# Performance work log

Hardware: AMD Instinct MI355X
Metric: run time of the kernel (lower is better)

## Reference

```python
import jax, jax.numpy as jnp
import numpy as np


def setup_inputs() -> dict:
    key = jax.random.key(0)
    ks = jax.random.split(key, 6)
    B, H, W, C = 4, 64, 64, 256
    D = 256 // 4  # inter_channel // 4
    return {
        "g": jax.random.normal(ks[0], (B, H, W, C), dtype=jnp.float32),
        "x": jax.random.normal(ks[1], (B, H, W, C), dtype=jnp.float32),
        "x_query": jax.random.normal(ks[2], (B, H, W, D), dtype=jnp.float32),
        "phi_g": jax.random.normal(ks[3], (B, H, W, D), dtype=jnp.float32),
        "x_value": jax.random.normal(ks[4], (B, H, W, C), dtype=jnp.float32),
        "k": jax.random.normal(ks[5], (1,), dtype=jnp.float32),
    }


def reference(g, x, x_query, phi_g, x_value, k):
    B, H, W, C = x.shape
    D = x_query.shape[-1]
    HW = H * W
    q = x_query.reshape(B, HW, D)
    pg = phi_g.reshape(B, HW, D)
    v = x_value.reshape(B, HW, C)
    # scale[b,i,j] = sum_d phi_g[b,i,d] * x_query[b,j,d]  -> (B, HW, HW)
    scale = jnp.einsum("bid,bjd->bij", pg, q)
    soft = jax.nn.softmax(scale, axis=-1)
    # scaled_value[b,i,c] = sum_j soft[b,i,j] * v[b,j,c]
    sv = jnp.einsum("bij,bjc->bic", soft, v).reshape(B, H, W, C)
    layero = k * sv + x
    return jnp.concatenate([layero, g], axis=3)
```

## Files before the change

kernel.cpp:

```cpp
#include <hip/hip_runtime.h>

#define N_  4096
#define D_  64
#define C_  256

typedef short bf16x8 __attribute__((ext_vector_type(8)));
typedef float f32x4  __attribute__((ext_vector_type(4)));

__device__ __forceinline__ unsigned short f2bf(float f) {
    union { float f; unsigned int i; } v; v.f = f;
    unsigned int r = v.i + 0x7fffu + ((v.i >> 16) & 1u);
    return (unsigned short)(r >> 16);
}

__global__ void prepass_kernel(const float* __restrict__ xq,
                               const float* __restrict__ pg,
                               const float* __restrict__ xv,
                               unsigned short* __restrict__ qbf,
                               unsigned short* __restrict__ pgbf,
                               unsigned short* __restrict__ vt2) {
    const int bid = blockIdx.x;
    const int t   = threadIdx.x;
    if (bid < 512) {
        const float* src = (bid < 256) ? xq : pg;
        unsigned short* dst = (bid < 256) ? qbf : pgbf;
        const int base = (bid & 255) * 1024 + t;
#pragma unroll
        for (int it = 0; it < 4; ++it) {
            const int i = base + it * 256;
            float4 v = ((const float4*)src)[i];
            ushort4 o;
            o.x = f2bf(v.x); o.y = f2bf(v.y); o.z = f2bf(v.z); o.w = f2bf(v.w);
            ((ushort4*)dst)[i] = o;
        }
        return;
    }
    const int lane = t & 63;
    const int w    = t >> 6;
    const int l15  = lane & 15;
    const int quad = lane >> 4;
    const int f    = (bid - 512) * 4 + w;
    const int b    = f >> 11;
    const int jt   = (f >> 6) & 31;
    const int cb   = (f >> 2) & 15;
    const int ks   = f & 3;
    const int c    = cb * 16 + l15;
    const int jb   = jt * 128 + ks * 32 + quad * 8;
    const float* src = xv + ((size_t)b * N_ + jb) * C_ + c;
    float v0 = src[0 * C_], v1 = src[1 * C_], v2 = src[2 * C_], v3 = src[3 * C_];
    float v4 = src[4 * C_], v5 = src[5 * C_], v6 = src[6 * C_], v7 = src[7 * C_];
    uint4 o;
    o.x = (unsigned)f2bf(v0) | ((unsigned)f2bf(v1) << 16);
    o.y = (unsigned)f2bf(v2) | ((unsigned)f2bf(v3) << 16);
    o.z = (unsigned)f2bf(v4) | ((unsigned)f2bf(v5) << 16);
    o.w = (unsigned)f2bf(v6) | ((unsigned)f2bf(v7) << 16);
    *(uint4*)(vt2 + (size_t)f * 512 + lane * 8) = o;
}

__global__ __launch_bounds__(512, 2) void attn_main(
    const float* __restrict__ g,  const float* __restrict__ x,
    const float* __restrict__ kk, float* __restrict__ out,
    const unsigned short* __restrict__ qbf,
    const unsigned short* __restrict__ pgbf,
    const unsigned short* __restrict__ vt2)
{
    __shared__ unsigned short p_lds[2][64 * 128];
    __shared__ float s_l[64];

    const int t    = threadIdx.x;
    const int lane = t & 63;
    const int w    = t >> 6;
    const int l15  = lane & 15;
    const int quad = lane >> 4;
    const int swz  = (l15 & 7) << 4;

    const int bid = blockIdx.x;
    const int b   = bid & 3;
    const int rg  = bid >> 2;
    const int i0  = rg * 64;
    const size_t rowbase = (size_t)b * N_ + i0;

    if (t < 64) s_l[t] = 0.f;

#pragma unroll
    for (int it = 0; it < 8; ++it) {
        const int row = it * 8 + w;
        const int c4  = lane * 4;
        const float4 gv = *(const float4*)(g + (rowbase + row) * C_ + c4);
        *(float4*)(out + (rowbase + row) * (2 * C_) + C_ + c4) = gv;
    }

    bf16x8 pgf[4][2];
#pragma unroll
    for (int nt = 0; nt < 4; ++nt)
#pragma unroll
        for (int ks = 0; ks < 2; ++ks)
            pgf[nt][ks] = *(const bf16x8*)(pgbf +
                (rowbase + nt * 16 + l15) * D_ + ks * 32 + quad * 8);

    f32x4 oacc[4][2];
#pragma unroll
    for (int mt = 0; mt < 4; ++mt) { oacc[mt][0] = (f32x4){0.f,0.f,0.f,0.f};
                                     oacc[mt][1] = (f32x4){0.f,0.f,0.f,0.f}; }
    float ls[4] = {0.f, 0.f, 0.f, 0.f};

    const unsigned short* qb  = qbf + (size_t)b * N_ * D_;
    const unsigned short* vtb = vt2 + (size_t)b * N_ * C_;
    unsigned short* const pb0 = &p_lds[0][0];
    unsigned short* const pb1 = &p_lds[1][0];

    auto load_q = [&](bf16x8 (&qf)[2], int jt) {
#pragma unroll
        for (int ks = 0; ks < 2; ++ks)
            qf[ks] = *(const bf16x8*)(qb +
                (size_t)(jt * 128 + w * 16 + l15) * D_ + ks * 32 + quad * 8);
    };
    auto load_v = [&](bf16x8 (&vf)[4][2], int jt) {
        const unsigned short* tbase = vtb + (size_t)jt * 32768;
#pragma unroll
        for (int ks = 0; ks < 4; ++ks)
#pragma unroll
            for (int ctl = 0; ctl < 2; ++ctl)
                vf[ks][ctl] = *(const bf16x8*)(tbase +
                    (size_t)(((w * 2 + ctl) * 4) + ks) * 512 + lane * 8);
    };
    auto s_step = [&](const bf16x8 (&qf)[2], unsigned short* pbuf) {
        f32x4 sacc[4];
#pragma unroll
        for (int nt = 0; nt < 4; ++nt) sacc[nt] = (f32x4){0.f,0.f,0.f,0.f};
#pragma unroll
        for (int ks = 0; ks < 2; ++ks)
#pragma unroll
            for (int nt = 0; nt < 4; ++nt)
                sacc[nt] = __builtin_amdgcn_mfma_f32_16x16x32_bf16(
                    qf[ks], pgf[nt][ks], sacc[nt], 0, 0, 0);
#pragma unroll
        for (int nt = 0; nt < 4; ++nt) {
            const float p0 = __expf(sacc[nt][0]);
            const float p1 = __expf(sacc[nt][1]);
            const float p2 = __expf(sacc[nt][2]);
            const float p3 = __expf(sacc[nt][3]);
            ls[nt] += (p0 + p1) + (p2 + p3);
            ushort4 pk;
            pk.x = f2bf(p0); pk.y = f2bf(p1); pk.z = f2bf(p2); pk.w = f2bf(p3);
            const int wb = ((nt * 16 + l15) * 256 + (w * 16 + quad * 4) * 2) ^ swz;
            *(ushort4*)((char*)pbuf + wb) = pk;
        }
    };
    auto pv_step = [&](const bf16x8 (&vf)[4][2], const unsigned short* pbuf) {
#pragma unroll
        for (int ks = 0; ks < 4; ++ks) {
            bf16x8 pa[4];
#pragma unroll
            for (int mt = 0; mt < 4; ++mt) {
                const int rb = ((mt * 16 + l15) * 256 + (ks * 32 + quad * 8) * 2) ^ swz;
                pa[mt] = *(const bf16x8*)((const char*)pbuf + rb);
            }
#pragma unroll
            for (int mt = 0; mt < 4; ++mt) {
                oacc[mt][0] = __builtin_amdgcn_mfma_f32_16x16x32_bf16(pa[mt], vf[ks][0], oacc[mt][0], 0, 0, 0);
                oacc[mt][1] = __builtin_amdgcn_mfma_f32_16x16x32_bf16(pa[mt], vf[ks][1], oacc[mt][1], 0, 0, 0);
            }
        }
    };

    bf16x8 qfA[2], qfB[2], vfA[4][2], vfB[4][2];

    load_q(qfA, 0);
    load_v(vfA, 0);
    s_step(qfA, pb0);
    load_q(qfB, 1);
    __syncthreads();

#pragma unroll 1
    for (int jtp = 0; jtp < 15; ++jtp) {
        const int jt0 = 2 * jtp;
        load_v(vfB, jt0 + 1);
        load_q(qfA, jt0 + 2);
        s_step(qfB, pb1);
        pv_step(vfA, pb0);
        __syncthreads();
        load_v(vfA, jt0 + 2);
        load_q(qfB, jt0 + 3);
        s_step(qfA, pb0);
        pv_step(vfB, pb1);
        __syncthreads();
    }
    load_v(vfB, 31);
    s_step(qfB, pb1);
    pv_step(vfA, pb0);
    __syncthreads();
    pv_step(vfB, pb1);

#pragma unroll
    for (int nt = 0; nt < 4; ++nt) {
        float s = ls[nt];
        s += __shfl_xor(s, 16);
        s += __shfl_xor(s, 32);
        if (lane < 16) atomicAdd(&s_l[nt * 16 + lane], s);
    }
    __syncthreads();

    const float kval = kk[0];
#pragma unroll
    for (int mt = 0; mt < 4; ++mt)
#pragma unroll
        for (int r = 0; r < 4; ++r) {
            const int m = mt * 16 + quad * 4 + r;
            const float linv = 1.f / s_l[m];
            const size_t row = rowbase + m;
#pragma unroll
            for (int ctl = 0; ctl < 2; ++ctl) {
                const int c = w * 32 + ctl * 16 + l15;
                out[row * (2 * C_) + c] = kval * (oacc[mt][ctl][r] * linv) + x[row * C_ + c];
            }
        }
}

#define ROWS 4
#define FNT  256
__global__ __launch_bounds__(FNT, 2) void attn_fallback(
    const float* __restrict__ g, const float* __restrict__ x,
    const float* __restrict__ xq, const float* __restrict__ pg,
    const float* __restrict__ xv, const float* __restrict__ kk,
    float* __restrict__ out)
{
    __shared__ __align__(16) float s_pg[ROWS][D_];
    __shared__ __align__(16) float s_sc[N_ * ROWS];
    __shared__ float s_rmax[4][ROWS];
    __shared__ float s_rsum[4][ROWS];

    const int t = threadIdx.x, lane = t & 63, w = t >> 6, blk = blockIdx.x;
    const int b = blk >> 10, i0 = (blk & 1023) * ROWS;
    const size_t rowbase = (size_t)b * N_ + i0;
    {
        const int r = t >> 6, cc = (t & 63) * 4;
        const float4 gv = *(const float4*)(g + (rowbase + r) * C_ + cc);
        *(float4*)(out + (rowbase + r) * (2 * C_) + C_ + cc) = gv;
    }
    { const int r = t >> 6, d = t & 63; s_pg[r][d] = pg[(rowbase + r) * D_ + d]; }
    __syncthreads();
    const float* qb = xq + (size_t)b * N_ * D_;
    float lmax[ROWS];
#pragma unroll
    for (int r = 0; r < ROWS; ++r) lmax[r] = -1e30f;
    for (int jj = 0; jj < N_ / FNT; ++jj) {
        const int j = t + jj * FNT;
        const float4* q4p = (const float4*)(qb + (size_t)j * D_);
        float s[ROWS] = {0.f, 0.f, 0.f, 0.f};
#pragma unroll
        for (int u = 0; u < D_ / 8; ++u) {
            const float4 qa = q4p[u * 2], qc = q4p[u * 2 + 1];
#pragma unroll
            for (int r = 0; r < ROWS; ++r) {
                const float4 pa = *(const float4*)&s_pg[r][u * 8];
                const float4 pb = *(const float4*)&s_pg[r][u * 8 + 4];
                s[r] += qa.x * pa.x + qa.y * pa.y + qa.z * pa.z + qa.w * pa.w
                      + qc.x * pb.x + qc.y * pb.y + qc.z * pb.z + qc.w * pb.w;
            }
        }
        *(float4*)&s_sc[j * ROWS] = make_float4(s[0], s[1], s[2], s[3]);
#pragma unroll
        for (int r = 0; r < ROWS; ++r) lmax[r] = fmaxf(lmax[r], s[r]);
    }
#pragma unroll
    for (int r = 0; r < ROWS; ++r) {
        float m = lmax[r];
        for (int o = 32; o > 0; o >>= 1) m = fmaxf(m, __shfl_down(m, o));
        if (lane == 0) s_rmax[w][r] = m;
    }
    __syncthreads();
    float bmax[ROWS];
#pragma unroll
    for (int r = 0; r < ROWS; ++r)
        bmax[r] = fmaxf(fmaxf(s_rmax[0][r], s_rmax[1][r]), fmaxf(s_rmax[2][r], s_rmax[3][r]));
    float lsum[ROWS] = {0.f, 0.f, 0.f, 0.f};
    for (int jj = 0; jj < N_ / FNT; ++jj) {
        const int j = t + jj * FNT;
        float4 s4 = *(const float4*)&s_sc[j * ROWS];
        s4.x = __expf(s4.x - bmax[0]); s4.y = __expf(s4.y - bmax[1]);
        s4.z = __expf(s4.z - bmax[2]); s4.w = __expf(s4.w - bmax[3]);
        *(float4*)&s_sc[j * ROWS] = s4;
        lsum[0] += s4.x; lsum[1] += s4.y; lsum[2] += s4.z; lsum[3] += s4.w;
    }
#pragma unroll
    for (int r = 0; r < ROWS; ++r) {
        float sm = lsum[r];
        for (int o = 32; o > 0; o >>= 1) sm += __shfl_down(sm, o);
        if (lane == 0) s_rsum[w][r] = sm;
    }
    __syncthreads();
    float rinv[ROWS];
#pragma unroll
    for (int r = 0; r < ROWS; ++r)
        rinv[r] = 1.f / (s_rsum[0][r] + s_rsum[1][r] + s_rsum[2][r] + s_rsum[3][r]);
    const int jg = lane >> 4;
    const int c0 = (w * 16 + (lane & 15)) * 4;
    const float* vb = xv + (size_t)b * N_ * C_;
    float acc[ROWS][4];
#pragma unroll
    for (int r = 0; r < ROWS; ++r)
#pragma unroll
        for (int q = 0; q < 4; ++q) acc[r][q] = 0.f;
#pragma unroll 4
    for (int jj = 0; jj < N_ / 4; ++jj) {
        const int j = jj * 4 + jg;
        const float4 p4 = *(const float4*)&s_sc[j * ROWS];
        const float4 v4 = *(const float4*)(vb + (size_t)j * C_ + c0);
        acc[0][0] += p4.x * v4.x; acc[0][1] += p4.x * v4.y; acc[0][2] += p4.x * v4.z; acc[0][3] += p4.x * v4.w;
        acc[1][0] += p4.y * v4.x; acc[1][1] += p4.y * v4.y; acc[1][2] += p4.y * v4.z; acc[1][3] += p4.y * v4.w;
        acc[2][0] += p4.z * v4.x; acc[2][1] += p4.z * v4.y; acc[2][2] += p4.z * v4.z; acc[2][3] += p4.z * v4.w;
        acc[3][0] += p4.w * v4.x; acc[3][1] += p4.w * v4.y; acc[3][2] += p4.w * v4.z; acc[3][3] += p4.w * v4.w;
    }
#pragma unroll
    for (int r = 0; r < ROWS; ++r)
#pragma unroll
        for (int q = 0; q < 4; ++q) {
            acc[r][q] += __shfl_xor(acc[r][q], 16);
            acc[r][q] += __shfl_xor(acc[r][q], 32);
        }
    const float kval = kk[0];
    if (lane < 16) {
        const int c = (w * 16 + lane) * 4;
#pragma unroll
        for (int r = 0; r < ROWS; ++r) {
            const float4 xv4 = *(const float4*)(x + (rowbase + r) * C_ + c);
            float4 ov;
            ov.x = kval * (acc[r][0] * rinv[r]) + xv4.x;
            ov.y = kval * (acc[r][1] * rinv[r]) + xv4.y;
            ov.z = kval * (acc[r][2] * rinv[r]) + xv4.z;
            ov.w = kval * (acc[r][3] * rinv[r]) + xv4.w;
            *(float4*)(out + (rowbase + r) * (2 * C_) + c) = ov;
        }
    }
}

extern "C" void kernel_launch(void* const* d_in, const int* in_sizes, int n_in,
                              void* d_out, int out_size, void* d_ws, size_t ws_size,
                              hipStream_t stream) {
    const float* g  = (const float*)d_in[0];
    const float* x  = (const float*)d_in[1];
    const float* xq = (const float*)d_in[2];
    const float* pg = (const float*)d_in[3];
    const float* xv = (const float*)d_in[4];
    const float* kk = (const float*)d_in[5];
    float* out = (float*)d_out;

    const int B = in_sizes[0] / (N_ * C_);
    const size_t qn = (size_t)B * N_ * D_;
    const size_t vn = (size_t)B * N_ * C_;
    const size_t need = (2 * qn + vn) * sizeof(unsigned short);

    if (B != 4 || ws_size < need) {
        attn_fallback<<<dim3(B * (N_ / ROWS)), FNT, 0, stream>>>(g, x, xq, pg, xv, kk, out);
        return;
    }

    unsigned short* qbf  = (unsigned short*)d_ws;
    unsigned short* pgbf = qbf + qn;
    unsigned short* vt2  = pgbf + qn;

    prepass_kernel<<<dim3(512 + B * 512), 256, 0, stream>>>(xq, pg, xv, qbf, pgbf, vt2);
    attn_main<<<dim3(B * (N_ / 64)), 512, 0, stream>>>(g, x, kk, out, qbf, pgbf, vt2);
}
```

Baseline: 153.6 us.

## Split PV over key quarters per wave with wider C tiles and LDS reduction

Each wave now handles one quarter of the 128-key tile and half of the 256 output channels, so it issues a single P fragment read per mt and keeps 32 accumulators. The V tile is single-buffered instead of double-buffered. The goal is fewer LDS P reads per MFMA and better reuse of P fragments across channel tiles. The partial sums from the four key quarters are combined through a multi-stage LDS tree reduction (~140KB LDS), and the output store is vectorized to float4. This costs a large rise in accumulator register pressure and LDS use, which may drop occupancy below the 2-block launch bound, and V loads are no longer prefetched a stage ahead.

```diff
diff --git a/kernel.cpp b/kernel.cpp
--- a/kernel.cpp
+++ b/kernel.cpp
@@ -64,7 +64,7 @@
     const unsigned short* __restrict__ pgbf,
     const unsigned short* __restrict__ vt2)
 {
-    __shared__ unsigned short p_lds[2][64 * 128];
+    __shared__ __align__(16) unsigned char smem[143360];
     __shared__ float s_l[64];
 
     const int t    = threadIdx.x;
@@ -73,6 +73,8 @@
     const int l15  = lane & 15;
     const int quad = lane >> 4;
     const int swz  = (l15 & 7) << 4;
+    const int jq   = w >> 1;
+    const int ch2  = w & 1;
 
     const int bid = blockIdx.x;
     const int b   = bid & 3;
@@ -98,16 +100,18 @@
             pgf[nt][ks] = *(const bf16x8*)(pgbf +
                 (rowbase + nt * 16 + l15) * D_ + ks * 32 + quad * 8);
 
-    f32x4 oacc[4][2];
-#pragma unroll
-    for (int mt = 0; mt < 4; ++mt) { oacc[mt][0] = (f32x4){0.f,0.f,0.f,0.f};
-                                     oacc[mt][1] = (f32x4){0.f,0.f,0.f,0.f}; }
+    f32x4 oacc[4][8];
+#pragma unroll
+    for (int mt = 0; mt < 4; ++mt)
+#pragma unroll
+        for (int ct = 0; ct < 8; ++ct)
+            oacc[mt][ct] = (f32x4){0.f, 0.f, 0.f, 0.f};
     float ls[4] = {0.f, 0.f, 0.f, 0.f};
 
     const unsigned short* qb  = qbf + (size_t)b * N_ * D_;
     const unsigned short* vtb = vt2 + (size_t)b * N_ * C_;
-    unsigned short* const pb0 = &p_lds[0][0];
-    unsigned short* const pb1 = &p_lds[1][0];
+    unsigned short* const pb0 = (unsigned short*)smem;
+    unsigned short* const pb1 = (unsigned short*)(smem + 32768);
 
     auto load_q = [&](bf16x8 (&qf)[2], int jt) {
 #pragma unroll
@@ -115,14 +119,12 @@
             qf[ks] = *(const bf16x8*)(qb +
                 (size_t)(jt * 128 + w * 16 + l15) * D_ + ks * 32 + quad * 8);
     };
-    auto load_v = [&](bf16x8 (&vf)[4][2], int jt) {
-        const unsigned short* tbase = vtb + (size_t)jt * 32768;
-#pragma unroll
-        for (int ks = 0; ks < 4; ++ks)
-#pragma unroll
-            for (int ctl = 0; ctl < 2; ++ctl)
-                vf[ks][ctl] = *(const bf16x8*)(tbase +
-                    (size_t)(((w * 2 + ctl) * 4) + ks) * 512 + lane * 8);
+    auto load_v = [&](bf16x8 (&vf)[8], int jt) {
+        const unsigned short* tbase = vtb +
+            ((size_t)(jt * 16 + ch2 * 8) * 4 + jq) * 512 + (size_t)lane * 8;
+#pragma unroll
+        for (int ct = 0; ct < 8; ++ct)
+            vf[ct] = *(const bf16x8*)(tbase + (size_t)ct * 2048);
     };
     auto s_step = [&](const bf16x8 (&qf)[2], unsigned short* pbuf) {
         f32x4 sacc[4];
@@ -147,50 +149,48 @@
             *(ushort4*)((char*)pbuf + wb) = pk;
         }
     };
-    auto pv_step = [&](const bf16x8 (&vf)[4][2], const unsigned short* pbuf) {
-#pragma unroll
-        for (int ks = 0; ks < 4; ++ks) {
-            bf16x8 pa[4];
-#pragma unroll
-            for (int mt = 0; mt < 4; ++mt) {
-                const int rb = ((mt * 16 + l15) * 256 + (ks * 32 + quad * 8) * 2) ^ swz;
-                pa[mt] = *(const bf16x8*)((const char*)pbuf + rb);
-            }
-#pragma unroll
-            for (int mt = 0; mt < 4; ++mt) {
-                oacc[mt][0] = __builtin_amdgcn_mfma_f32_16x16x32_bf16(pa[mt], vf[ks][0], oacc[mt][0], 0, 0, 0);
-                oacc[mt][1] = __builtin_amdgcn_mfma_f32_16x16x32_bf16(pa[mt], vf[ks][1], oacc[mt][1], 0, 0, 0);
-            }
-        }
+    auto pv_step = [&](const bf16x8 (&vf)[8], const unsigned short* pbuf) {
+        bf16x8 pa[4];
+#pragma unroll
+        for (int mt = 0; mt < 4; ++mt) {
+            const int rb = ((mt * 16 + l15) * 256 + jq * 64 + quad * 16) ^ swz;
+            pa[mt] = *(const bf16x8*)((const char*)pbuf + rb);
+        }
+#pragma unroll
+        for (int ct = 0; ct < 8; ++ct)
+#pragma unroll
+            for (int mt = 0; mt < 4; ++mt)
+                oacc[mt][ct] = __builtin_amdgcn_mfma_f32_16x16x32_bf16(
+                    pa[mt], vf[ct], oacc[mt][ct], 0, 0, 0);
     };
 
-    bf16x8 qfA[2], qfB[2], vfA[4][2], vfB[4][2];
+    bf16x8 qfA[2], qfB[2], vf[8];
 
     load_q(qfA, 0);
-    load_v(vfA, 0);
     s_step(qfA, pb0);
     load_q(qfB, 1);
     __syncthreads();
 
 #pragma unroll 1
     for (int jtp = 0; jtp < 15; ++jtp) {
-        const int jt0 = 2 * jtp;
-        load_v(vfB, jt0 + 1);
-        load_q(qfA, jt0 + 2);
+        const int p = 2 * jtp;
+        load_v(vf, p);
+        load_q(qfA, p + 2);
         s_step(qfB, pb1);
-        pv_step(vfA, pb0);
+        pv_step(vf, pb0);
         __syncthreads();
-        load_v(vfA, jt0 + 2);
-        load_q(qfB, jt0 + 3);
+        load_v(vf, p + 1);
+        load_q(qfB, p + 3);
         s_step(qfA, pb0);
-        pv_step(vfB, pb1);
+        pv_step(vf, pb1);
         __syncthreads();
     }
-    load_v(vfB, 31);
+    load_v(vf, 30);
     s_step(qfB, pb1);
-    pv_step(vfA, pb0);
-    __syncthreads();
-    pv_step(vfB, pb1);
+    pv_step(vf, pb0);
+    __syncthreads();
+    load_v(vf, 31);
+    pv_step(vf, pb1);
 
 #pragma unroll
     for (int nt = 0; nt < 4; ++nt) {
@@ -201,20 +201,75 @@
     }
     __syncthreads();
 
+    if (jq >= 2) {
+        float* Rg = (float*)(smem + (size_t)((jq - 2) * 2 + ch2) * 35840);
+#pragma unroll
+        for (int mt = 0; mt < 4; ++mt)
+#pragma unroll
+            for (int ct = 0; ct < 8; ++ct)
+#pragma unroll
+                for (int r = 0; r < 4; ++r)
+                    Rg[(mt * 16 + quad * 4 + r) * 140 + ct * 16 + l15] = oacc[mt][ct][r];
+    }
+    __syncthreads();
+    if (jq < 2) {
+        const float* Rg = (const float*)(smem + (size_t)(jq * 2 + ch2) * 35840);
+#pragma unroll
+        for (int mt = 0; mt < 4; ++mt)
+#pragma unroll
+            for (int ct = 0; ct < 8; ++ct)
+#pragma unroll
+                for (int r = 0; r < 4; ++r)
+                    oacc[mt][ct][r] += Rg[(mt * 16 + quad * 4 + r) * 140 + ct * 16 + l15];
+    }
+    __syncthreads();
+    if (jq == 1) {
+        float* Rg = (float*)(smem + (size_t)(0 * 2 + ch2) * 35840);
+#pragma unroll
+        for (int mt = 0; mt < 4; ++mt)
+#pragma unroll
+            for (int ct = 0; ct < 8; ++ct)
+#pragma unroll
+                for (int r = 0; r < 4; ++r)
+                    Rg[(mt * 16 + quad * 4 + r) * 140 + ct * 16 + l15] = oacc[mt][ct][r];
+    }
+    __syncthreads();
+    if (jq == 0) {
+        const float* Rg0 = (const float*)(smem + (size_t)(0 * 2 + ch2) * 35840);
+        float* Rg1 = (float*)(smem + (size_t)(1 * 2 + ch2) * 35840);
+#pragma unroll
+        for (int mt = 0; mt < 4; ++mt)
+#pragma unroll
+            for (int ct = 0; ct < 8; ++ct)
+#pragma unroll
+                for (int r = 0; r < 4; ++r) {
+                    const int idx = (mt * 16 + quad * 4 + r) * 140 + ct * 16 + l15;
+                    Rg1[idx] = oacc[mt][ct][r] + Rg0[idx];
+                }
+    }
+    __syncthreads();
+
     const float kval = kk[0];
-#pragma unroll
-    for (int mt = 0; mt < 4; ++mt)
-#pragma unroll
-        for (int r = 0; r < 4; ++r) {
-            const int m = mt * 16 + quad * 4 + r;
-            const float linv = 1.f / s_l[m];
-            const size_t row = rowbase + m;
-#pragma unroll
-            for (int ctl = 0; ctl < 2; ++ctl) {
-                const int c = w * 32 + ctl * 16 + l15;
-                out[row * (2 * C_) + c] = kval * (oacc[mt][ctl][r] * linv) + x[row * C_ + c];
-            }
-        }
+    const int row  = w * 8 + (lane >> 3);
+    const float linv = 1.f / s_l[row];
+    const size_t rr = rowbase + row;
+#pragma unroll
+    for (int b2 = 0; b2 < 2; ++b2) {
+        const float* Rf = (const float*)(smem + (size_t)(2 + b2) * 35840);
+#pragma unroll
+        for (int u = 0; u < 4; ++u) {
+            const int cl = (lane & 7) * 4 + u * 32;
+            const f32x4 ov = *(const f32x4*)&Rf[row * 140 + cl];
+            const int c = b2 * 128 + cl;
+            const float4 xv4 = *(const float4*)(x + rr * C_ + c);
+            float4 o4;
+            o4.x = kval * (ov[0] * linv) + xv4.x;
+            o4.y = kval * (ov[1] * linv) + xv4.y;
+            o4.z = kval * (ov[2] * linv) + xv4.z;
+            o4.w = kval * (ov[3] * linv) + xv4.w;
+            *(float4*)(out + rr * (2 * C_) + c) = o4;
+        }
+    }
 }
 
 #define ROWS 4
```

Result: slower. 184.9 us (+20.4%).

## Split PV work by key-half and channel quarter, reduce partials through LDS

Applied to the files above, without the earlier changes.

The PV MMA work is repartitioned. Each wave now covers 64 output channels over half of the key tile's k-steps, instead of 32 channels over all k-steps, so every P fragment read from LDS feeds four MFMAs instead of two. The two key-half partial accumulators are summed through a padded LDS buffer, and the epilogue writes output with coalesced float4 stores. In exchange the accumulator register count doubles (64 floats), LDS grows to about 68KB, and two extra barriers are added, which may reduce occupancy below the two blocks per CU requested.

```diff
diff --git a/kernel.cpp b/kernel.cpp
--- a/kernel.cpp
+++ b/kernel.cpp
@@ -64,7 +64,7 @@
     const unsigned short* __restrict__ pgbf,
     const unsigned short* __restrict__ vt2)
 {
-    __shared__ unsigned short p_lds[2][64 * 128];
+    __shared__ __align__(16) unsigned char smem[69632];
     __shared__ float s_l[64];
 
     const int t    = threadIdx.x;
@@ -73,6 +73,8 @@
     const int l15  = lane & 15;
     const int quad = lane >> 4;
     const int swz  = (l15 & 7) << 4;
+    const int jh   = w >> 2;
+    const int ch4  = w & 3;
 
     const int bid = blockIdx.x;
     const int b   = bid & 3;
@@ -98,16 +100,18 @@
             pgf[nt][ks] = *(const bf16x8*)(pgbf +
                 (rowbase + nt * 16 + l15) * D_ + ks * 32 + quad * 8);
 
-    f32x4 oacc[4][2];
-#pragma unroll
-    for (int mt = 0; mt < 4; ++mt) { oacc[mt][0] = (f32x4){0.f,0.f,0.f,0.f};
-                                     oacc[mt][1] = (f32x4){0.f,0.f,0.f,0.f}; }
+    f32x4 oacc[4][4];
+#pragma unroll
+    for (int mt = 0; mt < 4; ++mt)
+#pragma unroll
+        for (int ct = 0; ct < 4; ++ct)
+            oacc[mt][ct] = (f32x4){0.f, 0.f, 0.f, 0.f};
     float ls[4] = {0.f, 0.f, 0.f, 0.f};
 
     const unsigned short* qb  = qbf + (size_t)b * N_ * D_;
     const unsigned short* vtb = vt2 + (size_t)b * N_ * C_;
-    unsigned short* const pb0 = &p_lds[0][0];
-    unsigned short* const pb1 = &p_lds[1][0];
+    unsigned short* const pb0 = (unsigned short*)smem;
+    unsigned short* const pb1 = (unsigned short*)(smem + 16384);
 
     auto load_q = [&](bf16x8 (&qf)[2], int jt) {
 #pragma unroll
@@ -115,14 +119,14 @@
             qf[ks] = *(const bf16x8*)(qb +
                 (size_t)(jt * 128 + w * 16 + l15) * D_ + ks * 32 + quad * 8);
     };
-    auto load_v = [&](bf16x8 (&vf)[4][2], int jt) {
-        const unsigned short* tbase = vtb + (size_t)jt * 32768;
-#pragma unroll
-        for (int ks = 0; ks < 4; ++ks)
-#pragma unroll
-            for (int ctl = 0; ctl < 2; ++ctl)
-                vf[ks][ctl] = *(const bf16x8*)(tbase +
-                    (size_t)(((w * 2 + ctl) * 4) + ks) * 512 + lane * 8);
+    auto load_v = [&](bf16x8 (&vf)[2][4], int jt) {
+#pragma unroll
+        for (int ks2 = 0; ks2 < 2; ++ks2)
+#pragma unroll
+            for (int ct = 0; ct < 4; ++ct)
+                vf[ks2][ct] = *(const bf16x8*)(vtb +
+                    ((size_t)(jt * 16 + ch4 * 4 + ct) * 4 + (jh * 2 + ks2)) * 512 +
+                    (size_t)lane * 8);
     };
     auto s_step = [&](const bf16x8 (&qf)[2], unsigned short* pbuf) {
         f32x4 sacc[4];
@@ -147,24 +151,26 @@
             *(ushort4*)((char*)pbuf + wb) = pk;
         }
     };
-    auto pv_step = [&](const bf16x8 (&vf)[4][2], const unsigned short* pbuf) {
-#pragma unroll
-        for (int ks = 0; ks < 4; ++ks) {
+    auto pv_step = [&](const bf16x8 (&vf)[2][4], const unsigned short* pbuf) {
+#pragma unroll
+        for (int ks2 = 0; ks2 < 2; ++ks2) {
+            const int ks = jh * 2 + ks2;
             bf16x8 pa[4];
 #pragma unroll
             for (int mt = 0; mt < 4; ++mt) {
-                const int rb = ((mt * 16 + l15) * 256 + (ks * 32 + quad * 8) * 2) ^ swz;
+                const int rb = ((mt * 16 + l15) * 256 + ks * 64 + quad * 16) ^ swz;
                 pa[mt] = *(const bf16x8*)((const char*)pbuf + rb);
             }
 #pragma unroll
-            for (int mt = 0; mt < 4; ++mt) {
-                oacc[mt][0] = __builtin_amdgcn_mfma_f32_16x16x32_bf16(pa[mt], vf[ks][0], oacc[mt][0], 0, 0, 0);
-                oacc[mt][1] = __builtin_amdgcn_mfma_f32_16x16x32_bf16(pa[mt], vf[ks][1], oacc[mt][1], 0, 0, 0);
-            }
+            for (int ct = 0; ct < 4; ++ct)
+#pragma unroll
+                for (int mt = 0; mt < 4; ++mt)
+                    oacc[mt][ct] = __builtin_amdgcn_mfma_f32_16x16x32_bf16(
+                        pa[mt], vf[ks2][ct], oacc[mt][ct], 0, 0, 0);
         }
     };
 
-    bf16x8 qfA[2], qfB[2], vfA[4][2], vfB[4][2];
+    bf16x8 qfA[2], qfB[2], vfA[2][4], vfB[2][4];
 
     load_q(qfA, 0);
     load_v(vfA, 0);
@@ -174,14 +180,14 @@
 
 #pragma unroll 1
     for (int jtp = 0; jtp < 15; ++jtp) {
-        const int jt0 = 2 * jtp;
-        load_v(vfB, jt0 + 1);
-        load_q(qfA, jt0 + 2);
+        const int p = 2 * jtp;
+        load_v(vfB, p + 1);
+        load_q(qfA, p + 2);
         s_step(qfB, pb1);
         pv_step(vfA, pb0);
         __syncthreads();
-        load_v(vfA, jt0 + 2);
-        load_q(qfB, jt0 + 3);
+        load_v(vfA, p + 2);
+        load_q(qfB, p + 3);
         s_step(qfA, pb0);
         pv_step(vfB, pb1);
         __syncthreads();
@@ -201,20 +207,51 @@
     }
     __syncthreads();
 
+    {
+        float* Rg = (float*)(smem + (size_t)ch4 * 17408);
+        if (jh == 1) {
+#pragma unroll
+            for (int mt = 0; mt < 4; ++mt)
+#pragma unroll
+                for (int ct = 0; ct < 4; ++ct)
+#pragma unroll
+                    for (int r = 0; r < 4; ++r)
+                        Rg[(mt * 16 + quad * 4 + r) * 68 + ct * 16 + l15] = oacc[mt][ct][r];
+        }
+        __syncthreads();
+        if (jh == 0) {
+#pragma unroll
+            for (int mt = 0; mt < 4; ++mt)
+#pragma unroll
+                for (int ct = 0; ct < 4; ++ct)
+#pragma unroll
+                    for (int r = 0; r < 4; ++r) {
+                        const int idx = (mt * 16 + quad * 4 + r) * 68 + ct * 16 + l15;
+                        Rg[idx] += oacc[mt][ct][r];
+                    }
+        }
+        __syncthreads();
+    }
+
     const float kval = kk[0];
 #pragma unroll
-    for (int mt = 0; mt < 4; ++mt)
-#pragma unroll
-        for (int r = 0; r < 4; ++r) {
-            const int m = mt * 16 + quad * 4 + r;
-            const float linv = 1.f / s_l[m];
-            const size_t row = rowbase + m;
-#pragma unroll
-            for (int ctl = 0; ctl < 2; ++ctl) {
-                const int c = w * 32 + ctl * 16 + l15;
-                out[row * (2 * C_) + c] = kval * (oacc[mt][ctl][r] * linv) + x[row * C_ + c];
-            }
-        }
+    for (int it = 0; it < 8; ++it) {
+        const int idx = it * 512 + t;
+        const int row = idx >> 6;
+        const int cq  = idx & 63;
+        const int c   = cq * 4;
+        const float* Rg = (const float*)(smem + (size_t)(cq >> 4) * 17408);
+        const f32x4 ov = *(const f32x4*)&Rg[row * 68 + (cq & 15) * 4];
+        const float linv = 1.f / s_l[row];
+        const size_t rr = rowbase + row;
+        const float4 xv4 = *(const float4*)(x + rr * C_ + c);
+        float4 o4;
+        o4.x = kval * (ov[0] * linv) + xv4.x;
+        o4.y = kval * (ov[1] * linv) + xv4.y;
+        o4.z = kval * (ov[2] * linv) + xv4.z;
+        o4.w = kval * (ov[3] * linv) + xv4.w;
+        *(float4*)(out + rr * (2 * C_) + c) = o4;
+    }
 }
 
 #define ROWS 4
```

New measurement: 160.4 us. +4.4%, slower.
